# Kernel tuning notes

Measured on AMD Instinct MI355X. Metric: run time of the kernel, lower is better.

The kernel has to match this reference:

```python
import jax, jax.numpy as jnp
import numpy as np

B, T, D, H, L = 8192, 80, 32, 64, 3


def setup_inputs() -> dict:
    key = jax.random.key(0)
    ks = jax.random.split(key, 16)
    s = lambda k, shape, fan: jax.random.normal(k, shape, jnp.float32) / np.sqrt(fan)
    inp = {"x": jax.random.normal(ks[0], (B, T, D), jnp.float32)}
    dims_in = [D, H, H]
    i = 1
    for l in range(L):
        din = dims_in[l]
        inp[f"W_ih{l}"] = s(ks[i], (H, din), H); i += 1
        inp[f"W_hh{l}"] = s(ks[i], (H, H), H); i += 1
        inp[f"b_ih{l}"] = s(ks[i], (H,), H); i += 1
        inp[f"b_hh{l}"] = s(ks[i], (H,), H); i += 1
    inp["W_fc"] = s(ks[i], (1, H), H); i += 1
    inp["b_fc"] = s(ks[i], (1,), H)
    return inp


def _rnn_layer(xs, W_ih, W_hh, b_ih, b_hh):
    # xs: [T, B, Din] -> ys: [T, B, H]; tanh RNN recurrence (PyTorch nn.RNN math)
    pre = jnp.einsum('tbd,hd->tbh', xs, W_ih) + b_ih + b_hh  # input proj precomputed
    h0 = jnp.zeros((xs.shape[1], W_hh.shape[0]), xs.dtype)
    def step(h, p):
        h_new = jnp.tanh(p + h @ W_hh.T)
        return h_new, h_new
    _, ys = jax.lax.scan(step, h0, pre)
    return ys


def reference(x, W_ih0, W_hh0, b_ih0, b_hh0, W_ih1, W_hh1, b_ih1, b_hh1,
              W_ih2, W_hh2, b_ih2, b_hh2, W_fc, b_fc):
    # x: [B, T, D] (batch_first) -> time-major [T, B, D]
    h = jnp.swapaxes(x, 0, 1)
    params = [(W_ih0, W_hh0, b_ih0, b_hh0),
              (W_ih1, W_hh1, b_ih1, b_hh1),
              (W_ih2, W_hh2, b_ih2, b_hh2)]
    for (W_ih, W_hh, b_ih, b_hh) in params:
        h = _rnn_layer(h, W_ih, W_hh, b_ih, b_hh)
    last = h[-1]                      # [B, H] == out[:, -1, :]
    return last @ W_fc.T + b_fc       # [B, 1]
```

## Files before the change

kernel.cpp:

```cpp
#include <hip/hip_runtime.h>
#include <hip/hip_bf16.h>
#include <cstddef>


typedef __attribute__((ext_vector_type(8))) short s16x8;
typedef __attribute__((ext_vector_type(4))) short s16x4;
typedef __attribute__((ext_vector_type(4))) float fx4;

#define MFMA32(A, B, C) __builtin_amdgcn_mfma_f32_16x16x32_bf16((A), (B), (C), 0, 0, 0)
#define MFMA16(A, B, C) __builtin_amdgcn_mfma_f32_16x16x16bf16_1k((A), (B), (C), 0, 0, 0)

#if __has_builtin(__builtin_amdgcn_exp2f)
#define EXP2F(x) __builtin_amdgcn_exp2f(x)
#else
#define EXP2F(x) exp2f(x)
#endif
#if __has_builtin(__builtin_amdgcn_rcpf)
#define RCPF(x) __builtin_amdgcn_rcpf(x)
#else
#define RCPF(x) (1.0f / (x))
#endif

static constexpr float K2LOG2E = 2.8853900817779268f;

__device__ __forceinline__ short f2bf(float f) {
  union { float f; unsigned u; } v; v.f = f;
  unsigned r = v.u + 0x7FFFu + ((v.u >> 16) & 1u);
  return (short)(r >> 16);
}
__device__ __forceinline__ float bf2f(short s) {
  union { unsigned u; float f; } v; v.u = ((unsigned)(unsigned short)s) << 16;
  return v.f;
}
__device__ __forceinline__ unsigned pk2bf(float a, float b) {
  float2 t; t.x = a; t.y = b;
  union { __hip_bfloat162 h; unsigned u; } c;
  c.h = __float22bfloat162_rn(t);
  return c.u;
}

__device__ __forceinline__ s16x4 wfragA16(const float* W, int ncols, int row, int col0) {
  const float* p = W + row * ncols + col0;
  s16x4 r;
#pragma unroll
  for (int i = 0; i < 4; ++i) r[i] = f2bf(p[i]);
  return r;
}
__device__ __forceinline__ s16x8 wfragA32(const float* W, int ncols, int row, int col0) {
  const float* p = W + row * ncols + col0;
  s16x8 r;
#pragma unroll
  for (int i = 0; i < 8; ++i) r[i] = f2bf(p[i]);
  return r;
}

__device__ __forceinline__ s16x4 tanh_pack(fx4 acc, const float* bs) {
  float h[4];
#pragma unroll
  for (int r = 0; r < 4; ++r) {
    float e = EXP2F(__builtin_fmaf(acc[r], K2LOG2E, bs[r]));
    h[r] = __builtin_fmaf(-2.f, RCPF(e + 1.f), 1.f);
  }
  union { unsigned u[2]; s16x4 v; } p;
  p.u[0] = pk2bf(h[0], h[1]);
  p.u[1] = pk2bf(h[2], h[3]);
  return p.v;
}

__global__ __launch_bounds__(192, 2) void rnn3_chunk4b(
    const float* __restrict__ x,
    const float* __restrict__ Wih0, const float* __restrict__ Whh0,
    const float* __restrict__ bih0, const float* __restrict__ bhh0,
    const float* __restrict__ Wih1, const float* __restrict__ Whh1,
    const float* __restrict__ bih1, const float* __restrict__ bhh1,
    const float* __restrict__ Wih2, const float* __restrict__ Whh2,
    const float* __restrict__ bih2, const float* __restrict__ bhh2,
    const float* __restrict__ Wfc, const float* __restrict__ bfc,
    float* __restrict__ out)
{
  __shared__ __align__(16) short hb[2][8][16][72];

  const int tid = threadIdx.x;
  const int wv  = __builtin_amdgcn_readfirstlane(tid >> 6);
  const int ln  = tid & 63;
  const int q   = ln >> 4;
  const int m15 = ln & 15;
  const int bbase = (int)blockIdx.x * 16;

  const float* Wih = (wv == 0) ? Wih0 : (wv == 1) ? Wih1 : Wih2;
  const float* Whh = (wv == 0) ? Whh0 : (wv == 1) ? Whh1 : Whh2;
  const float* bi  = (wv == 0) ? bih0 : (wv == 1) ? bih1 : bih2;
  const float* bh  = (wv == 0) ? bhh0 : (wv == 1) ? bhh1 : bhh2;
  const int kin = (wv == 0) ? 32 : 64;

  s16x8 wiA[4], wiB[4];
  s16x4 wh16[4][4];
  const s16x8 z8 = {0, 0, 0, 0, 0, 0, 0, 0};
#pragma unroll
  for (int t4 = 0; t4 < 4; ++t4) {
    const int row = 16 * t4 + m15;
    wiA[t4] = wfragA32(Wih, kin, row, 8 * q);
    wiB[t4] = wv ? wfragA32(Wih, 64, row, 32 + 8 * q) : z8;
#pragma unroll
    for (int kf = 0; kf < 4; ++kf)
      wh16[t4][kf] = wfragA16(Whh, 64, row, 16 * kf + 4 * q);
  }

  float bsc[4][4];
#pragma unroll
  for (int t4 = 0; t4 < 4; ++t4)
#pragma unroll
    for (int r = 0; r < 4; ++r) {
      const int j = 16 * t4 + 4 * q + r;
      bsc[t4][r] = (bi[j] + bh[j]) * K2LOG2E;
    }

  const fx4 z4 = {0.f, 0.f, 0.f, 0.f};
  const s16x4 z2 = {0, 0, 0, 0};
  s16x4 hf[4] = {z2, z2, z2, z2};

  const float* xr = x + (size_t)(bbase + m15) * (80 * 32) + 8 * q;
  fx4 xb0[4], xb1[4];
  if (wv == 0) {
#pragma unroll
    for (int jj = 0; jj < 4; ++jj) {
      xb0[jj] = *(const fx4*)(xr + jj * 32);
      xb1[jj] = *(const fx4*)(xr + jj * 32 + 4);
    }
  }

  for (int m = 0; m < 22; ++m) {
    const int lt0 = 4 * (m - wv);
    if (0 <= lt0 && lt0 <= 76) {
      s16x8 inA[4], inB[4];
      if (wv == 0) {
#pragma unroll
        for (int jj = 0; jj < 4; ++jj) {
          union { unsigned u[4]; s16x8 v; } xp;
          xp.u[0] = pk2bf(xb0[jj][0], xb0[jj][1]);
          xp.u[1] = pk2bf(xb0[jj][2], xb0[jj][3]);
          xp.u[2] = pk2bf(xb1[jj][0], xb1[jj][1]);
          xp.u[3] = pk2bf(xb1[jj][2], xb1[jj][3]);
          inA[jj] = xp.v; inB[jj] = z8;
        }
#pragma unroll
        for (int jj = 0; jj < 4; ++jj) {
          const int tt = (lt0 + 4 + jj <= 79) ? lt0 + 4 + jj : 79;
          xb0[jj] = *(const fx4*)(xr + tt * 32);
          xb1[jj] = *(const fx4*)(xr + tt * 32 + 4);
        }
      } else {
#pragma unroll
        for (int jj = 0; jj < 4; ++jj) {
          const short* up = &hb[wv - 1][(lt0 + jj) & 7][m15][8 * q];
          inA[jj] = *(const s16x8*)(up);
          inB[jj] = *(const s16x8*)(up + 32);
        }
      }
      fx4 acc[4][4];
#pragma unroll
      for (int jj = 0; jj < 4; ++jj)
#pragma unroll
        for (int t4 = 0; t4 < 4; ++t4) acc[jj][t4] = MFMA32(wiA[t4], inA[jj], z4);
      if (wv) {
#pragma unroll
        for (int jj = 0; jj < 4; ++jj)
#pragma unroll
          for (int t4 = 0; t4 < 4; ++t4)
            acc[jj][t4] = MFMA32(wiB[t4], inB[jj], acc[jj][t4]);
      }
#pragma unroll
      for (int jj = 0; jj < 4; ++jj) {
        const int st = (lt0 + jj) & 7;
#pragma unroll
        for (int kf = 0; kf < 4; ++kf)
#pragma unroll
          for (int t4 = 0; t4 < 4; ++t4)
            acc[jj][t4] = MFMA16(wh16[t4][kf], hf[kf], acc[jj][t4]);
        short* wb = &hb[wv & 1][st][m15][4 * q];
#pragma unroll
        for (int t4 = 0; t4 < 4; ++t4) {
          s16x4 hv = tanh_pack(acc[jj][t4], bsc[t4]);
          hf[t4] = hv;
          if (wv != 2) *(s16x4*)(wb + 16 * t4) = hv;
        }
      }
    }
    __syncthreads();
  }

  if (wv == 2) {
    float sv = 0.f;
#pragma unroll
    for (int kf = 0; kf < 4; ++kf)
#pragma unroll
      for (int i = 0; i < 4; ++i)
        sv += bf2f(hf[kf][i]) * Wfc[16 * kf + 4 * q + i];
    sv += __shfl_xor(sv, 16, 64);
    sv += __shfl_xor(sv, 32, 64);
    if (ln < 16) out[bbase + ln] = sv + bfc[0];
  }
}

extern "C" void kernel_launch(void* const* d_in, const int* in_sizes, int n_in,
                              void* d_out, int out_size, void* d_ws, size_t ws_size,
                              hipStream_t stream) {
  const float* x    = (const float*)d_in[0];
  const float* Wih0 = (const float*)d_in[1];
  const float* Whh0 = (const float*)d_in[2];
  const float* bih0 = (const float*)d_in[3];
  const float* bhh0 = (const float*)d_in[4];
  const float* Wih1 = (const float*)d_in[5];
  const float* Whh1 = (const float*)d_in[6];
  const float* bih1 = (const float*)d_in[7];
  const float* bhh1 = (const float*)d_in[8];
  const float* Wih2 = (const float*)d_in[9];
  const float* Whh2 = (const float*)d_in[10];
  const float* bih2 = (const float*)d_in[11];
  const float* bhh2 = (const float*)d_in[12];
  const float* Wfc  = (const float*)d_in[13];
  const float* bfc  = (const float*)d_in[14];

  rnn3_chunk4b<<<dim3(512), dim3(192), 0, stream>>>(
      x, Wih0, Whh0, bih0, bhh0, Wih1, Whh1, bih1, bhh1,
      Wih2, Whh2, bih2, bhh2, Wfc, bfc, (float*)d_out);
}
```

Before: 194.5 us.

## Widen wavefront-pipelined chunks to six timesteps and split recurrent MFMA chain

Each wavefront (one per layer) now handles six timesteps per barrier round instead of four, cutting the outer loop from 22 to 16 iterations and so the number of __syncthreads. The shared-memory ring grows to 12 slots, used as two alternating halves, and partial final chunks are guarded. The input projection is now computed per timestep inside the loop rather than batched up front. The recurrent h@W_hh product is split into two independent MFMA accumulation chains summed before tanh, which shortens the dependent chain on the serial critical path. The costs are a longer pipeline fill/drain (each layer lags by six steps), more registers and shared memory, and conditional branches on the tail.

Measured after the change: 206.8 us. +6.3%, slower.

```diff
diff --git a/kernel.cpp b/kernel.cpp
--- a/kernel.cpp
+++ b/kernel.cpp
@@ -67,7 +67,7 @@
   return p.v;
 }
 
-__global__ __launch_bounds__(192, 2) void rnn3_chunk4b(
+__global__ __launch_bounds__(192, 2) void rnn3_chunk6(
     const float* __restrict__ x,
     const float* __restrict__ Wih0, const float* __restrict__ Whh0,
     const float* __restrict__ bih0, const float* __restrict__ bhh0,
@@ -78,7 +78,7 @@
     const float* __restrict__ Wfc, const float* __restrict__ bfc,
     float* __restrict__ out)
 {
-  __shared__ __align__(16) short hb[2][8][16][72];
+  __shared__ __align__(16) short hb[2][12][16][72];
 
   const int tid = threadIdx.x;
   const int wv  = __builtin_amdgcn_readfirstlane(tid >> 6);
@@ -120,69 +120,74 @@
   s16x4 hf[4] = {z2, z2, z2, z2};
 
   const float* xr = x + (size_t)(bbase + m15) * (80 * 32) + 8 * q;
-  fx4 xb0[4], xb1[4];
+  fx4 xb0[6], xb1[6];
   if (wv == 0) {
 #pragma unroll
-    for (int jj = 0; jj < 4; ++jj) {
+    for (int jj = 0; jj < 6; ++jj) {
       xb0[jj] = *(const fx4*)(xr + jj * 32);
       xb1[jj] = *(const fx4*)(xr + jj * 32 + 4);
     }
   }
 
-  for (int m = 0; m < 22; ++m) {
-    const int lt0 = 4 * (m - wv);
-    if (0 <= lt0 && lt0 <= 76) {
-      s16x8 inA[4], inB[4];
+  for (int m = 0; m < 16; ++m) {
+    const int k   = m - wv;
+    const int lt0 = 6 * k;
+    if (0 <= lt0 && lt0 <= 79) {
+      const int base = (k & 1) * 6;
+      s16x8 inA[6], inB[6];
+#pragma unroll
+      for (int jj = 0; jj < 6; ++jj) { inA[jj] = z8; inB[jj] = z8; }
       if (wv == 0) {
 #pragma unroll
-        for (int jj = 0; jj < 4; ++jj) {
+        for (int jj = 0; jj < 6; ++jj) {
           union { unsigned u[4]; s16x8 v; } xp;
           xp.u[0] = pk2bf(xb0[jj][0], xb0[jj][1]);
           xp.u[1] = pk2bf(xb0[jj][2], xb0[jj][3]);
           xp.u[2] = pk2bf(xb1[jj][0], xb1[jj][1]);
           xp.u[3] = pk2bf(xb1[jj][2], xb1[jj][3]);
-          inA[jj] = xp.v; inB[jj] = z8;
-        }
-#pragma unroll
-        for (int jj = 0; jj < 4; ++jj) {
-          const int tt = (lt0 + 4 + jj <= 79) ? lt0 + 4 + jj : 79;
+          inA[jj] = xp.v;
+        }
+#pragma unroll
+        for (int jj = 0; jj < 6; ++jj) {
+          const int tt = (lt0 + 6 + jj <= 79) ? lt0 + 6 + jj : 79;
           xb0[jj] = *(const fx4*)(xr + tt * 32);
           xb1[jj] = *(const fx4*)(xr + tt * 32 + 4);
         }
       } else {
 #pragma unroll
-        for (int jj = 0; jj < 4; ++jj) {
-          const short* up = &hb[wv - 1][(lt0 + jj) & 7][m15][8 * q];
-          inA[jj] = *(const s16x8*)(up);
-          inB[jj] = *(const s16x8*)(up + 32);
+        for (int jj = 0; jj < 6; ++jj) {
+          if (lt0 + jj <= 79) {
+            const short* up = &hb[wv - 1][base + jj][m15][8 * q];
+            inA[jj] = *(const s16x8*)(up);
+            inB[jj] = *(const s16x8*)(up + 32);
+          }
         }
       }
-      fx4 acc[4][4];
-#pragma unroll
-      for (int jj = 0; jj < 4; ++jj)
-#pragma unroll
-        for (int t4 = 0; t4 < 4; ++t4) acc[jj][t4] = MFMA32(wiA[t4], inA[jj], z4);
-      if (wv) {
-#pragma unroll
-        for (int jj = 0; jj < 4; ++jj)
-#pragma unroll
-          for (int t4 = 0; t4 < 4; ++t4)
-            acc[jj][t4] = MFMA32(wiB[t4], inB[jj], acc[jj][t4]);
-      }
-#pragma unroll
-      for (int jj = 0; jj < 4; ++jj) {
-        const int st = (lt0 + jj) & 7;
-#pragma unroll
-        for (int kf = 0; kf < 4; ++kf)
-#pragma unroll
-          for (int t4 = 0; t4 < 4; ++t4)
-            acc[jj][t4] = MFMA16(wh16[t4][kf], hf[kf], acc[jj][t4]);
-        short* wb = &hb[wv & 1][st][m15][4 * q];
-#pragma unroll
-        for (int t4 = 0; t4 < 4; ++t4) {
-          s16x4 hv = tanh_pack(acc[jj][t4], bsc[t4]);
-          hf[t4] = hv;
-          if (wv != 2) *(s16x4*)(wb + 16 * t4) = hv;
+#pragma unroll
+      for (int jj = 0; jj < 6; ++jj) {
+        if (lt0 + jj <= 79) {
+          fx4 ae[4], ao[4];
+#pragma unroll
+          for (int t4 = 0; t4 < 4; ++t4) ae[t4] = MFMA32(wiA[t4], inA[jj], z4);
+          if (wv) {
+#pragma unroll
+            for (int t4 = 0; t4 < 4; ++t4) ae[t4] = MFMA32(wiB[t4], inB[jj], ae[t4]);
+          }
+#pragma unroll
+          for (int t4 = 0; t4 < 4; ++t4) ao[t4] = MFMA16(wh16[t4][1], hf[1], z4);
+#pragma unroll
+          for (int t4 = 0; t4 < 4; ++t4) ae[t4] = MFMA16(wh16[t4][0], hf[0], ae[t4]);
+#pragma unroll
+          for (int t4 = 0; t4 < 4; ++t4) ao[t4] = MFMA16(wh16[t4][3], hf[3], ao[t4]);
+#pragma unroll
+          for (int t4 = 0; t4 < 4; ++t4) ae[t4] = MFMA16(wh16[t4][2], hf[2], ae[t4]);
+          short* wb = &hb[wv & 1][base + jj][m15][4 * q];
+#pragma unroll
+          for (int t4 = 0; t4 < 4; ++t4) {
+            s16x4 hv = tanh_pack(ae[t4] + ao[t4], bsc[t4]);
+            hf[t4] = hv;
+            if (wv != 2) *(s16x4*)(wb + 16 * t4) = hv;
+          }
         }
       }
     }
@@ -221,7 +226,7 @@
   const float* Wfc  = (const float*)d_in[13];
   const float* bfc  = (const float*)d_in[14];
 
-  rnn3_chunk4b<<<dim3(512), dim3(192), 0, stream>>>(
+  rnn3_chunk6<<<dim3(512), dim3(192), 0, stream>>>(
       x, Wih0, Whh0, bih0, bhh0, Wih1, Whh1, bih1, bhh1,
       Wih2, Whh2, bih2, bhh2, Wfc, bfc, (float*)d_out);
 }
```
